# Optimization experiments

Measured on AMD Instinct MI355X. Metric: run time of the kernel, lower is better.

Reference implementation:

```python
import jax, jax.numpy as jnp
import numpy as np

K = 2            # top-k experts
TEMP = 1.0       # temperature
LN_EPS = 1e-5

def setup_inputs() -> dict:
    key = jax.random.key(0)
    B, S, D, E = 4, 4096, 2048, 64
    k0, k1, k2, k3 = jax.random.split(key, 4)
    x = jax.random.normal(k0, (B, S, D), dtype=jnp.float32)
    Wg = jax.random.normal(k1, (E, D), dtype=jnp.float32) * 0.02       # base_gate weight [out,in]
    gamma = jnp.ones((D,), jnp.float32)                                 # LayerNorm weight
    beta = jnp.zeros((D,), jnp.float32)                                 # LayerNorm bias
    W1 = jax.random.normal(k2, (D // 2, D), dtype=jnp.float32) * 0.02   # diff_pred linear1
    W2 = jax.random.normal(k3, (1, D // 2), dtype=jnp.float32) * 0.02   # diff_pred linear2
    return {"x": x, "Wg": Wg, "gamma": gamma, "beta": beta, "W1": W1, "W2": W2}

def reference(x, Wg, gamma, beta, W1, W2):
    # base expert logits: [B,S,E]
    logits = jnp.einsum('bsd,ed->bse', x, Wg)
    # difficulty predictor: LN -> Linear -> GELU -> Linear -> sigmoid, [B,S,1]
    mu = jnp.mean(x, axis=-1, keepdims=True)
    var = jnp.var(x, axis=-1, keepdims=True)
    h = (x - mu) * jax.lax.rsqrt(var + LN_EPS) * gamma + beta
    h1 = jax.nn.gelu(jnp.einsum('bsd,hd->bsh', h, W1), approximate=False)
    diff = jax.nn.sigmoid(jnp.einsum('bsh,oh->bso', h1, W2))
    # modulate + temperature (eval mode: no jitter / mask_drop)
    logits = logits / (1.0 + diff) * (1.0 / TEMP)
    probs_soft = jax.nn.softmax(logits, axis=-1)
    # top-k selection
    _, idx = jax.lax.top_k(logits, K)                    # [B,S,K]
    hard_any = jnp.max(jax.nn.one_hot(idx, logits.shape[-1], dtype=probs_soft.dtype), axis=2)  # [B,S,E]
    probs_st = hard_any - probs_soft + probs_soft        # faithful to source (no detach)
    scores = jnp.take_along_axis(probs_st, idx, axis=-1)  # [B,S,K]
    scores = scores / jnp.maximum(jnp.sum(scores, axis=-1, keepdims=True), 1e-9)
    importance = jax.lax.stop_gradient(jnp.mean(probs_soft, axis=(0, 1)))  # [E]
    load = jax.lax.stop_gradient(jnp.mean(hard_any, axis=(0, 1)))          # [E]
    return (idx, scores, probs_soft, importance, load)
```

## Files before the change

kernel.cpp:

```cpp
#include <hip/hip_runtime.h>
#include <math.h>

#define BS_TOK 16384
#define DIM    2048
#define NEXP   64
#define DHID   1024
#define GKS    4
#define KSL    (DIM / GKS)

typedef __attribute__((ext_vector_type(8))) _Float16 f16x8;
typedef __attribute__((ext_vector_type(4))) float    f32x4;

#define GLOBAL_AS const __attribute__((address_space(1))) void*
#define LDS_AS    __attribute__((address_space(3))) void*

__device__ __forceinline__ float gelu_f(float x) {
  return 0.5f * x * (1.0f + erff(x * 0.70710678118654752440f));
}

__global__ __launch_bounds__(256) void ln_kernel(const float* __restrict__ X,
                                                 const float* __restrict__ gamma,
                                                 const float* __restrict__ beta,
                                                 _Float16* __restrict__ H) {
  const int tid  = threadIdx.x;
  const int w    = tid >> 6, lane = tid & 63;
  const int t    = blockIdx.x * 4 + w;
  const float* xr = X + (size_t)t * DIM;
  float4 xv[8];
#pragma unroll
  for (int j = 0; j < 4; ++j) {
    const int c0 = (j * 64 + lane) * 8;
    xv[j * 2]     = *(const float4*)(xr + c0);
    xv[j * 2 + 1] = *(const float4*)(xr + c0 + 4);
  }
  float s = 0.f, q = 0.f;
#pragma unroll
  for (int j = 0; j < 8; ++j) {
    s += (xv[j].x + xv[j].y) + (xv[j].z + xv[j].w);
    q += (xv[j].x * xv[j].x + xv[j].y * xv[j].y) + (xv[j].z * xv[j].z + xv[j].w * xv[j].w);
  }
#pragma unroll
  for (int off = 32; off > 0; off >>= 1) {
    s += __shfl_xor(s, off);
    q += __shfl_xor(q, off);
  }
  const float mu  = s * (1.0f / DIM);
  const float var = q * (1.0f / DIM) - mu * mu;
  const float rs  = rsqrtf(var + 1e-5f);
#pragma unroll
  for (int j = 0; j < 4; ++j) {
    const int c0 = (j * 64 + lane) * 8;
    const float4 g0 = *(const float4*)(gamma + c0);
    const float4 g1 = *(const float4*)(gamma + c0 + 4);
    const float4 b0 = *(const float4*)(beta + c0);
    const float4 b1 = *(const float4*)(beta + c0 + 4);
    const float4 a = xv[j * 2], b = xv[j * 2 + 1];
    f16x8 h;
    h[0] = (_Float16)((a.x - mu) * rs * g0.x + b0.x);
    h[1] = (_Float16)((a.y - mu) * rs * g0.y + b0.y);
    h[2] = (_Float16)((a.z - mu) * rs * g0.z + b0.z);
    h[3] = (_Float16)((a.w - mu) * rs * g0.w + b0.w);
    h[4] = (_Float16)((b.x - mu) * rs * g1.x + b1.x);
    h[5] = (_Float16)((b.y - mu) * rs * g1.y + b1.y);
    h[6] = (_Float16)((b.z - mu) * rs * g1.z + b1.z);
    h[7] = (_Float16)((b.w - mu) * rs * g1.w + b1.w);
    *(f16x8*)(H + (size_t)t * DIM + c0) = h;
  }
}

__global__ __launch_bounds__(256) void w1cast_kernel(const float* __restrict__ W1,
                                                     _Float16* __restrict__ W1h) {
  const int i = (blockIdx.x * 256 + threadIdx.x) * 8;
  const float4 a = *(const float4*)(W1 + i);
  const float4 b = *(const float4*)(W1 + i + 4);
  f16x8 o;
  o[0] = (_Float16)a.x; o[1] = (_Float16)a.y; o[2] = (_Float16)a.z; o[3] = (_Float16)a.w;
  o[4] = (_Float16)b.x; o[5] = (_Float16)b.y; o[6] = (_Float16)b.z; o[7] = (_Float16)b.w;
  *(f16x8*)(W1h + i) = o;
}

#define GT_M 128
#define PX   132
#define PW   68
__global__ __launch_bounds__(128) void gate_kernel(const float* __restrict__ X,
                                                   const float* __restrict__ Wg,
                                                   float* __restrict__ logitsP) {
  __shared__ float sX[16][PX];
  __shared__ float sW[16][PW];
  const int tid  = threadIdx.x;
  const int m0   = blockIdx.x * GT_M;
  const int k0   = blockIdx.y * KSL;
  const int srow = tid >> 2;
  const int skq  = tid & 3;
  const int ty   = tid >> 3;
  const int tx   = tid & 7;
  const float* xb = X  + (size_t)(m0 + srow) * DIM + k0 + skq * 4;
  const float* wb = Wg + (size_t)srow * DIM + k0 + skq * 4;
  float acc[8][8] = {};
  float4 rx[4], rw[2];
#pragma unroll
  for (int r = 0; r < 4; ++r) rx[r] = *(const float4*)(xb + (size_t)(r * 32) * DIM);
#pragma unroll
  for (int r = 0; r < 2; ++r) rw[r] = *(const float4*)(wb + (size_t)(r * 32) * DIM);
  for (int kt = 0; kt < KSL; kt += 16) {
    __syncthreads();
#pragma unroll
    for (int r = 0; r < 4; ++r) {
      sX[skq * 4 + 0][srow + r * 32] = rx[r].x;
      sX[skq * 4 + 1][srow + r * 32] = rx[r].y;
      sX[skq * 4 + 2][srow + r * 32] = rx[r].z;
      sX[skq * 4 + 3][srow + r * 32] = rx[r].w;
    }
#pragma unroll
    for (int r = 0; r < 2; ++r) {
      sW[skq * 4 + 0][srow + r * 32] = rw[r].x;
      sW[skq * 4 + 1][srow + r * 32] = rw[r].y;
      sW[skq * 4 + 2][srow + r * 32] = rw[r].z;
      sW[skq * 4 + 3][srow + r * 32] = rw[r].w;
    }
    const int ktn = (kt + 16 < KSL) ? kt + 16 : 0;
#pragma unroll
    for (int r = 0; r < 4; ++r) rx[r] = *(const float4*)(xb + (size_t)(r * 32) * DIM + ktn);
#pragma unroll
    for (int r = 0; r < 2; ++r) rw[r] = *(const float4*)(wb + (size_t)(r * 32) * DIM + ktn);
    __syncthreads();
#pragma unroll
    for (int k = 0; k < 16; ++k) {
      const float4 a0 = *(const float4*)&sX[k][ty * 8];
      const float4 a1 = *(const float4*)&sX[k][ty * 8 + 4];
      const float4 b0 = *(const float4*)&sW[k][tx * 8];
      const float4 b1 = *(const float4*)&sW[k][tx * 8 + 4];
      const float av[8] = {a0.x, a0.y, a0.z, a0.w, a1.x, a1.y, a1.z, a1.w};
      const float bv[8] = {b0.x, b0.y, b0.z, b0.w, b1.x, b1.y, b1.z, b1.w};
#pragma unroll
      for (int i = 0; i < 8; ++i)
#pragma unroll
        for (int j = 0; j < 8; ++j) acc[i][j] += av[i] * bv[j];
    }
  }
  float* op = logitsP + (size_t)blockIdx.y * ((size_t)BS_TOK * NEXP)
            + (size_t)(m0 + ty * 8) * NEXP + tx * 8;
#pragma unroll
  for (int i = 0; i < 8; ++i) {
    float4 o0, o1;
    o0.x = acc[i][0]; o0.y = acc[i][1]; o0.z = acc[i][2]; o0.w = acc[i][3];
    o1.x = acc[i][4]; o1.y = acc[i][5]; o1.z = acc[i][6]; o1.w = acc[i][7];
    *(float4*)(op + (size_t)i * NEXP)     = o0;
    *(float4*)(op + (size_t)i * NEXP + 4) = o1;
  }
}

__global__ __launch_bounds__(256) void g2_kernel(const _Float16* __restrict__ H,
                                                 const _Float16* __restrict__ W1h,
                                                 const float* __restrict__ W2,
                                                 float* __restrict__ diffz) {
  __shared__ __align__(16) _Float16 sA[2][128 * 32];
  __shared__ __align__(16) _Float16 sB[2][128 * 32];
  const int bid = blockIdx.x;
  const int c   = bid & 7;
  const int j   = bid >> 3;
  const int m0  = (c * 16 + (j >> 3)) * 128;
  const int n0  = (j & 7) * 128;
  const int tid  = threadIdx.x;
  const int w    = tid >> 6, lane = tid & 63;
  const int wr   = w >> 1,  wc   = w & 1;
  const int col  = lane & 15, quad = lane >> 4;
  const int row0 = tid >> 2,  kp = tid & 3;
  const int row1 = row0 + 64;
  const _Float16* gA0 = H   + (size_t)(m0 + row0) * DIM + kp * 8;
  const _Float16* gA1 = H   + (size_t)(m0 + row1) * DIM + kp * 8;
  const _Float16* gB0 = W1h + (size_t)(n0 + row0) * DIM + kp * 8;
  const _Float16* gB1 = W1h + (size_t)(n0 + row1) * DIM + kp * 8;
  f32x4 acc[4][4] = {};
#define G2_STAGE(buf, off)                                                                              \
  do {                                                                                                  \
    __builtin_amdgcn_global_load_lds((GLOBAL_AS)(gA0 + (off)), (LDS_AS)(sA[buf] + tid * 8), 16, 0, 0);  \
    __builtin_amdgcn_global_load_lds((GLOBAL_AS)(gA1 + (off)), (LDS_AS)(sA[buf] + (256 + tid) * 8), 16, 0, 0); \
    __builtin_amdgcn_global_load_lds((GLOBAL_AS)(gB0 + (off)), (LDS_AS)(sB[buf] + tid * 8), 16, 0, 0);  \
    __builtin_amdgcn_global_load_lds((GLOBAL_AS)(gB1 + (off)), (LDS_AS)(sB[buf] + (256 + tid) * 8), 16, 0, 0); \
  } while (0)
  G2_STAGE(0, 0);
  __syncthreads();
  int cur = 0;
  for (int kt = 0; kt < DIM; kt += 32) {
    if (kt + 32 < DIM) G2_STAGE(cur ^ 1, kt + 32);
    f16x8 af[4], bf[4];
#pragma unroll
    for (int mi = 0; mi < 4; ++mi)
      af[mi] = *(const f16x8*)(sA[cur] + (wr * 64 + mi * 16 + col) * 32 + quad * 8);
#pragma unroll
    for (int ni = 0; ni < 4; ++ni)
      bf[ni] = *(const f16x8*)(sB[cur] + (wc * 64 + ni * 16 + col) * 32 + quad * 8);
#pragma unroll
    for (int mi = 0; mi < 4; ++mi)
#pragma unroll
      for (int ni = 0; ni < 4; ++ni)
        acc[mi][ni] = __builtin_amdgcn_mfma_f32_16x16x32_f16(af[mi], bf[ni], acc[mi][ni], 0, 0, 0);
    __syncthreads();
    cur ^= 1;
  }
  float w2v[4];
#pragma unroll
  for (int ni = 0; ni < 4; ++ni) w2v[ni] = W2[n0 + wc * 64 + ni * 16 + col];
#pragma unroll
  for (int mi = 0; mi < 4; ++mi) {
#pragma unroll
    for (int reg = 0; reg < 4; ++reg) {
      float v = 0.f;
#pragma unroll
      for (int ni = 0; ni < 4; ++ni) v += gelu_f(acc[mi][ni][reg]) * w2v[ni];
      v += __shfl_xor(v, 1);
      v += __shfl_xor(v, 2);
      v += __shfl_xor(v, 4);
      v += __shfl_xor(v, 8);
      if (col == 0)
        atomicAdd(diffz + m0 + wr * 64 + mi * 16 + quad * 4 + reg, v);
    }
  }
}

__global__ __launch_bounds__(256) void finalize_kernel(const float* __restrict__ logitsP,
                                                       const float* __restrict__ diffz,
                                                       float* __restrict__ out_idx,
                                                       float* __restrict__ out_scores,
                                                       float* __restrict__ out_probs,
                                                       float* __restrict__ imp_acc,
                                                       float* __restrict__ load_acc) {
  const int tid  = threadIdx.x;
  const int w    = tid >> 6, lane = tid & 63;
  const size_t PS = (size_t)BS_TOK * NEXP;
  float acc_imp = 0.f, acc_load = 0.f;
  for (int it = 0; it < 8; ++it) {
    const int t    = blockIdx.x * 32 + it * 4 + w;
    const float* lp = logitsP + (size_t)t * NEXP + lane;
    const float L  = ((lp[0] + lp[PS]) + lp[2 * PS]) + lp[3 * PS];
    const float z  = diffz[t];
    const float d  = 1.0f / (1.0f + expf(-z));
    const float l  = L / (1.0f + d);
    float m = l;
#pragma unroll
    for (int off = 32; off > 0; off >>= 1) m = fmaxf(m, __shfl_xor(m, off));
    float p = expf(l - m);
    float s = p;
#pragma unroll
    for (int off = 32; off > 0; off >>= 1) s += __shfl_xor(s, off);
    p /= s;
    float v = l; int bi = lane;
#pragma unroll
    for (int off = 32; off > 0; off >>= 1) {
      const float ov = __shfl_xor(v, off);
      const int   oi = __shfl_xor(bi, off);
      if (ov > v || (ov == v && oi < bi)) { v = ov; bi = oi; }
    }
    const int i1 = bi;
    float v2 = (lane == i1) ? -INFINITY : l;
    int bi2 = lane;
#pragma unroll
    for (int off = 32; off > 0; off >>= 1) {
      const float ov = __shfl_xor(v2, off);
      const int   oi = __shfl_xor(bi2, off);
      if (ov > v2 || (ov == v2 && oi < bi2)) { v2 = ov; bi2 = oi; }
    }
    const int i2 = bi2;
    const float p1 = __shfl(p, i1);
    const float p2 = __shfl(p, i2);
    const float s1 = (1.0f - p1) + p1;
    const float s2 = (1.0f - p2) + p2;
    const float den = fmaxf(s1 + s2, 1e-9f);
    if (lane == 0) {
      out_idx[t * 2]        = (float)i1;
      out_idx[t * 2 + 1]    = (float)i2;
      out_scores[t * 2]     = s1 / den;
      out_scores[t * 2 + 1] = s2 / den;
    }
    out_probs[(size_t)t * NEXP + lane] = p;
    acc_imp  += p;
    acc_load += (lane == i1 || lane == i2) ? 1.0f : 0.0f;
  }
  __shared__ float s_imp[256];
  __shared__ float s_hard[256];
  s_imp[tid]  = acc_imp;
  s_hard[tid] = acc_load;
  __syncthreads();
  if (tid < 64) {
    const float si = s_imp[tid] + s_imp[64 + tid] + s_imp[128 + tid] + s_imp[192 + tid];
    const float sl = s_hard[tid] + s_hard[64 + tid] + s_hard[128 + tid] + s_hard[192 + tid];
    atomicAdd(imp_acc + tid, si);
    atomicAdd(load_acc + tid, sl);
  }
}

__global__ void scale_kernel(const float* __restrict__ acc,
                             float* __restrict__ out_imp,
                             float* __restrict__ out_load) {
  const int tid = threadIdx.x;
  const float inv = 1.0f / 16384.0f;
  if (tid < 64)       out_imp[tid]        = acc[tid] * inv;
  else if (tid < 128) out_load[tid - 64]  = acc[tid] * inv;
}

extern "C" void kernel_launch(void* const* d_in, const int* in_sizes, int n_in,
                              void* d_out, int out_size, void* d_ws, size_t ws_size,
                              hipStream_t stream) {
  (void)in_sizes; (void)n_in; (void)out_size; (void)ws_size;
  const float* X     = (const float*)d_in[0];
  const float* Wg    = (const float*)d_in[1];
  const float* gamma = (const float*)d_in[2];
  const float* beta  = (const float*)d_in[3];
  const float* W1    = (const float*)d_in[4];
  const float* W2    = (const float*)d_in[5];
  float* out = (float*)d_out;

  char* ws = (char*)d_ws;
  _Float16* H       = (_Float16*)(ws);
  _Float16* W1h     = (_Float16*)(ws + 67108864ull);
  float*    logitsP = (float*)  (ws + 71303168ull);
  float*    diffz   = (float*)  (ws + 88080384ull);
  float*    accs    = (float*)  (ws + 88145920ull);

  float* out_idx    = out;
  float* out_scores = out + 32768;
  float* out_probs  = out + 65536;
  float* out_imp    = out + 1114112;
  float* out_load   = out + 1114176;

  hipMemsetAsync(diffz, 0, 65536ull + 512ull, stream);
  ln_kernel<<<BS_TOK / 4, 256, 0, stream>>>(X, gamma, beta, H);
  w1cast_kernel<<<(DHID * DIM) / (256 * 8), 256, 0, stream>>>(W1, W1h);
  gate_kernel<<<dim3(BS_TOK / GT_M, GKS), 128, 0, stream>>>(X, Wg, logitsP);
  g2_kernel<<<(DHID / 128) * (BS_TOK / 128), 256, 0, stream>>>(H, W1h, W2, diffz);
  finalize_kernel<<<BS_TOK / 32, 256, 0, stream>>>(logitsP, diffz, out_idx, out_scores,
                                                   out_probs, accs, accs + 64);
  scale_kernel<<<1, 128, 0, stream>>>(accs, out_imp, out_load);
}
```

Measured before the change: 430.9 us.

## Enlarge FFN GEMM tiles to 256x256x64 with swizzled LDS and 512 threads

The difficulty-predictor GEMM moves from 128x128x32 tiles with 256 threads to 256x256x64 tiles with 512 threads. It adds an XOR swizzle on LDS columns to avoid bank conflicts, interleaves MFMA with barriers and s_setprio, and remaps blocks to XCDs. The gate GEMM also moves to 256-row tiles with 256 threads and is launched before the LN kernel. Larger tiles cut global and LDS traffic per FLOP, at the cost of fewer blocks (256) and much higher LDS and register pressure.

```diff
diff --git a/kernel.cpp b/kernel.cpp
--- a/kernel.cpp
+++ b/kernel.cpp
@@ -79,10 +79,10 @@
   *(f16x8*)(W1h + i) = o;
 }
 
-#define GT_M 128
-#define PX   132
+#define GT_M 256
+#define PX   260
 #define PW   68
-__global__ __launch_bounds__(128) void gate_kernel(const float* __restrict__ X,
+__global__ __launch_bounds__(256) void gate_kernel(const float* __restrict__ X,
                                                    const float* __restrict__ Wg,
                                                    float* __restrict__ logitsP) {
   __shared__ float sX[16][PX];
@@ -97,32 +97,27 @@
   const float* xb = X  + (size_t)(m0 + srow) * DIM + k0 + skq * 4;
   const float* wb = Wg + (size_t)srow * DIM + k0 + skq * 4;
   float acc[8][8] = {};
-  float4 rx[4], rw[2];
-#pragma unroll
-  for (int r = 0; r < 4; ++r) rx[r] = *(const float4*)(xb + (size_t)(r * 32) * DIM);
-#pragma unroll
-  for (int r = 0; r < 2; ++r) rw[r] = *(const float4*)(wb + (size_t)(r * 32) * DIM);
+  float4 rx[4], rw;
+#pragma unroll
+  for (int g = 0; g < 4; ++g) rx[g] = *(const float4*)(xb + (size_t)(g * 64) * DIM);
+  rw = *(const float4*)wb;
   for (int kt = 0; kt < KSL; kt += 16) {
     __syncthreads();
 #pragma unroll
-    for (int r = 0; r < 4; ++r) {
-      sX[skq * 4 + 0][srow + r * 32] = rx[r].x;
-      sX[skq * 4 + 1][srow + r * 32] = rx[r].y;
-      sX[skq * 4 + 2][srow + r * 32] = rx[r].z;
-      sX[skq * 4 + 3][srow + r * 32] = rx[r].w;
-    }
-#pragma unroll
-    for (int r = 0; r < 2; ++r) {
-      sW[skq * 4 + 0][srow + r * 32] = rw[r].x;
-      sW[skq * 4 + 1][srow + r * 32] = rw[r].y;
-      sW[skq * 4 + 2][srow + r * 32] = rw[r].z;
-      sW[skq * 4 + 3][srow + r * 32] = rw[r].w;
-    }
+    for (int g = 0; g < 4; ++g) {
+      sX[skq * 4 + 0][srow + g * 64] = rx[g].x;
+      sX[skq * 4 + 1][srow + g * 64] = rx[g].y;
+      sX[skq * 4 + 2][srow + g * 64] = rx[g].z;
+      sX[skq * 4 + 3][srow + g * 64] = rx[g].w;
+    }
+    sW[skq * 4 + 0][srow] = rw.x;
+    sW[skq * 4 + 1][srow] = rw.y;
+    sW[skq * 4 + 2][srow] = rw.z;
+    sW[skq * 4 + 3][srow] = rw.w;
     const int ktn = (kt + 16 < KSL) ? kt + 16 : 0;
 #pragma unroll
-    for (int r = 0; r < 4; ++r) rx[r] = *(const float4*)(xb + (size_t)(r * 32) * DIM + ktn);
-#pragma unroll
-    for (int r = 0; r < 2; ++r) rw[r] = *(const float4*)(wb + (size_t)(r * 32) * DIM + ktn);
+    for (int g = 0; g < 4; ++g) rx[g] = *(const float4*)(xb + (size_t)(g * 64) * DIM + ktn);
+    rw = *(const float4*)(wb + ktn);
     __syncthreads();
 #pragma unroll
     for (int k = 0; k < 16; ++k) {
@@ -150,60 +145,92 @@
   }
 }
 
-__global__ __launch_bounds__(256) void g2_kernel(const _Float16* __restrict__ H,
-                                                 const _Float16* __restrict__ W1h,
-                                                 const float* __restrict__ W2,
-                                                 float* __restrict__ diffz) {
-  __shared__ __align__(16) _Float16 sA[2][128 * 32];
-  __shared__ __align__(16) _Float16 sB[2][128 * 32];
+#define G2BM 256
+#define G2BN 256
+#define G2BK 64
+#define G2NT (DIM / G2BK)
+
+__global__ __launch_bounds__(512, 2) void g2_kernel(const _Float16* __restrict__ H,
+                                                    const _Float16* __restrict__ W1h,
+                                                    const float* __restrict__ W2,
+                                                    float* __restrict__ diffz) {
+  __shared__ __align__(16) _Float16 sA[2][G2BM * G2BK];
+  __shared__ __align__(16) _Float16 sB[2][G2BN * G2BK];
   const int bid = blockIdx.x;
-  const int c   = bid & 7;
-  const int j   = bid >> 3;
-  const int m0  = (c * 16 + (j >> 3)) * 128;
-  const int n0  = (j & 7) * 128;
+  const int xcd = bid & 7;
+  const int loc = bid >> 3;
+  const int m0  = (xcd * 8 + (loc >> 2)) * G2BM;
+  const int n0  = (loc & 3) * G2BN;
   const int tid  = threadIdx.x;
-  const int w    = tid >> 6, lane = tid & 63;
-  const int wr   = w >> 1,  wc   = w & 1;
+  const int lane = tid & 63;
+  const int w    = tid >> 6;
+  const int wr   = w >> 2, wc = w & 3;
   const int col  = lane & 15, quad = lane >> 4;
-  const int row0 = tid >> 2,  kp = tid & 3;
-  const int row1 = row0 + 64;
-  const _Float16* gA0 = H   + (size_t)(m0 + row0) * DIM + kp * 8;
-  const _Float16* gA1 = H   + (size_t)(m0 + row1) * DIM + kp * 8;
-  const _Float16* gB0 = W1h + (size_t)(n0 + row0) * DIM + kp * 8;
-  const _Float16* gB1 = W1h + (size_t)(n0 + row1) * DIM + kp * 8;
-  f32x4 acc[4][4] = {};
-#define G2_STAGE(buf, off)                                                                              \
-  do {                                                                                                  \
-    __builtin_amdgcn_global_load_lds((GLOBAL_AS)(gA0 + (off)), (LDS_AS)(sA[buf] + tid * 8), 16, 0, 0);  \
-    __builtin_amdgcn_global_load_lds((GLOBAL_AS)(gA1 + (off)), (LDS_AS)(sA[buf] + (256 + tid) * 8), 16, 0, 0); \
-    __builtin_amdgcn_global_load_lds((GLOBAL_AS)(gB0 + (off)), (LDS_AS)(sB[buf] + tid * 8), 16, 0, 0);  \
-    __builtin_amdgcn_global_load_lds((GLOBAL_AS)(gB1 + (off)), (LDS_AS)(sB[buf] + (256 + tid) * 8), 16, 0, 0); \
+  const int c0   = col & 7;
+  const int srow8 = tid >> 3;
+  const int ksw   = (tid & 7) ^ (srow8 & 7);
+  const _Float16* gA = H   + (size_t)(m0 + srow8) * DIM + ksw * 8;
+  const _Float16* gB = W1h + (size_t)(n0 + srow8) * DIM + ksw * 8;
+  f32x4 acc[8][4] = {};
+#define G2_STAGE(bf_, kt_)                                                                          \
+  do {                                                                                              \
+    __builtin_amdgcn_global_load_lds((GLOBAL_AS)(gA + (kt_)),                 (LDS_AS)(sA[bf_] + tid * 8), 16, 0, 0);          \
+    __builtin_amdgcn_global_load_lds((GLOBAL_AS)(gA + (size_t)64  * DIM + (kt_)), (LDS_AS)(sA[bf_] + 4096 + tid * 8), 16, 0, 0);   \
+    __builtin_amdgcn_global_load_lds((GLOBAL_AS)(gA + (size_t)128 * DIM + (kt_)), (LDS_AS)(sA[bf_] + 8192 + tid * 8), 16, 0, 0);   \
+    __builtin_amdgcn_global_load_lds((GLOBAL_AS)(gA + (size_t)192 * DIM + (kt_)), (LDS_AS)(sA[bf_] + 12288 + tid * 8), 16, 0, 0);  \
+    __builtin_amdgcn_global_load_lds((GLOBAL_AS)(gB + (kt_)),                 (LDS_AS)(sB[bf_] + tid * 8), 16, 0, 0);          \
+    __builtin_amdgcn_global_load_lds((GLOBAL_AS)(gB + (size_t)64  * DIM + (kt_)), (LDS_AS)(sB[bf_] + 4096 + tid * 8), 16, 0, 0);   \
+    __builtin_amdgcn_global_load_lds((GLOBAL_AS)(gB + (size_t)128 * DIM + (kt_)), (LDS_AS)(sB[bf_] + 8192 + tid * 8), 16, 0, 0);   \
+    __builtin_amdgcn_global_load_lds((GLOBAL_AS)(gB + (size_t)192 * DIM + (kt_)), (LDS_AS)(sB[bf_] + 12288 + tid * 8), 16, 0, 0);  \
   } while (0)
   G2_STAGE(0, 0);
-  __syncthreads();
+  asm volatile("s_waitcnt vmcnt(0)" ::: "memory");
+  __builtin_amdgcn_s_barrier();
   int cur = 0;
-  for (int kt = 0; kt < DIM; kt += 32) {
-    if (kt + 32 < DIM) G2_STAGE(cur ^ 1, kt + 32);
-    f16x8 af[4], bf[4];
-#pragma unroll
-    for (int mi = 0; mi < 4; ++mi)
-      af[mi] = *(const f16x8*)(sA[cur] + (wr * 64 + mi * 16 + col) * 32 + quad * 8);
-#pragma unroll
-    for (int ni = 0; ni < 4; ++ni)
-      bf[ni] = *(const f16x8*)(sB[cur] + (wc * 64 + ni * 16 + col) * 32 + quad * 8);
-#pragma unroll
-    for (int mi = 0; mi < 4; ++mi)
+  for (int t = 0; t < G2NT; ++t) {
+    if (t + 1 < G2NT) G2_STAGE(cur ^ 1, (t + 1) * G2BK);
+    const _Float16* A = sA[cur];
+    const _Float16* B = sB[cur];
+    f16x8 af[4], bfr[4];
+#pragma unroll
+    for (int kh = 0; kh < 2; ++kh) {
+      const int sqz = ((kh * 4 + quad) ^ c0) * 8;
 #pragma unroll
       for (int ni = 0; ni < 4; ++ni)
-        acc[mi][ni] = __builtin_amdgcn_mfma_f32_16x16x32_f16(af[mi], bf[ni], acc[mi][ni], 0, 0, 0);
-    __syncthreads();
+        bfr[ni] = *(const f16x8*)(B + (wc * 64 + ni * 16 + col) * G2BK + sqz);
+#pragma unroll
+      for (int mi = 0; mi < 4; ++mi)
+        af[mi] = *(const f16x8*)(A + (wr * 128 + mi * 16 + col) * G2BK + sqz);
+      __builtin_amdgcn_s_setprio(1);
+#pragma unroll
+      for (int mi = 0; mi < 4; ++mi)
+#pragma unroll
+        for (int ni = 0; ni < 4; ++ni)
+          acc[mi][ni] = __builtin_amdgcn_mfma_f32_16x16x32_f16(af[mi], bfr[ni], acc[mi][ni], 0, 0, 0);
+      __builtin_amdgcn_s_setprio(0);
+      __builtin_amdgcn_s_barrier();
+#pragma unroll
+      for (int mi = 0; mi < 4; ++mi)
+        af[mi] = *(const f16x8*)(A + (wr * 128 + (mi + 4) * 16 + col) * G2BK + sqz);
+      __builtin_amdgcn_s_setprio(1);
+#pragma unroll
+      for (int mi = 0; mi < 4; ++mi)
+#pragma unroll
+        for (int ni = 0; ni < 4; ++ni)
+          acc[mi + 4][ni] = __builtin_amdgcn_mfma_f32_16x16x32_f16(af[mi], bfr[ni], acc[mi + 4][ni], 0, 0, 0);
+      __builtin_amdgcn_s_setprio(0);
+      __builtin_amdgcn_s_barrier();
+    }
+    if (t + 1 < G2NT) asm volatile("s_waitcnt vmcnt(0)" ::: "memory");
+    __builtin_amdgcn_s_barrier();
     cur ^= 1;
   }
+#undef G2_STAGE
   float w2v[4];
 #pragma unroll
   for (int ni = 0; ni < 4; ++ni) w2v[ni] = W2[n0 + wc * 64 + ni * 16 + col];
 #pragma unroll
-  for (int mi = 0; mi < 4; ++mi) {
+  for (int mi = 0; mi < 8; ++mi) {
 #pragma unroll
     for (int reg = 0; reg < 4; ++reg) {
       float v = 0.f;
@@ -214,7 +241,7 @@
       v += __shfl_xor(v, 4);
       v += __shfl_xor(v, 8);
       if (col == 0)
-        atomicAdd(diffz + m0 + wr * 64 + mi * 16 + quad * 4 + reg, v);
+        atomicAdd(diffz + m0 + wr * 128 + mi * 16 + quad * 4 + reg, v);
     }
   }
 }
@@ -325,10 +352,10 @@
   float* out_load   = out + 1114176;
 
   hipMemsetAsync(diffz, 0, 65536ull + 512ull, stream);
+  gate_kernel<<<dim3(BS_TOK / GT_M, GKS), 256, 0, stream>>>(X, Wg, logitsP);
   ln_kernel<<<BS_TOK / 4, 256, 0, stream>>>(X, gamma, beta, H);
   w1cast_kernel<<<(DHID * DIM) / (256 * 8), 256, 0, stream>>>(W1, W1h);
-  gate_kernel<<<dim3(BS_TOK / GT_M, GKS), 128, 0, stream>>>(X, Wg, logitsP);
-  g2_kernel<<<(DHID / 128) * (BS_TOK / 128), 256, 0, stream>>>(H, W1h, W2, diffz);
+  g2_kernel<<<(DHID / G2BN) * (BS_TOK / G2BM), 512, 0, stream>>>(H, W1h, W2, diffz);
   finalize_kernel<<<BS_TOK / 32, 256, 0, stream>>>(logitsP, diffz, out_idx, out_scores,
                                                    out_probs, accs, accs + 64);
   scale_kernel<<<1, 128, 0, stream>>>(accs, out_imp, out_load);
```

Measured after the change: 366.7 us. 1.17x faster.
